# Performance work log

Hardware: AMD Instinct MI355X
Metric: run time of the kernel (lower is better)

The kernel has to match this reference:

```python
import jax, jax.numpy as jnp
import numpy as np


def setup_inputs() -> dict:
    key = jax.random.key(0)
    k1, k2, k3 = jax.random.split(key, 3)
    B, Cin, H, W = 32, 128, 56, 56
    E, Cout = 8, 128
    x = jax.random.normal(k1, (B, Cin, H, W), dtype=jnp.float32)
    conv_w = jax.random.normal(k2, (E, Cout, Cin, 3, 3), dtype=jnp.float32) * 0.05
    gate_w = jax.random.normal(k3, (E, Cin), dtype=jnp.float32) * 0.05
    gate_b = jnp.zeros((E,), dtype=jnp.float32)
    return {"x": x, "conv_w": conv_w, "gate_w": gate_w, "gate_b": gate_b, "top_k": 2}


def reference(x, conv_w, gate_w, gate_b, top_k):
    # x: [B, Cin, H, W]; conv_w: [E, Cout, Cin, 3, 3]
    E, Cout, Cin, kh, kw = conv_w.shape
    B = x.shape[0]
    # Gate: global average pool -> linear logits over experts
    gap = x.mean(axis=(2, 3))                      # [B, Cin]
    logits = gap @ gate_w.T + gate_b               # [B, E]
    vals, idx = jax.lax.top_k(logits, top_k)       # [B, k]
    w = jax.nn.softmax(vals, axis=-1)              # renormalize over selected experts
    weights = jnp.zeros((B, E), dtype=x.dtype).at[jnp.arange(B)[:, None], idx].set(w)
    # All experts via a single conv with stacked output channels (stride=1, pad=1 == SAME)
    y = jax.lax.conv_general_dilated(
        x, conv_w.reshape(E * Cout, Cin, kh, kw),
        window_strides=(1, 1), padding='SAME',
        dimension_numbers=('NCHW', 'OIHW', 'NCHW'))  # [B, E*Cout, H, W]
    y = y.reshape(B, E, Cout, y.shape[2], y.shape[3])
    out = jnp.einsum('be,bechw->bchw', weights, y)  # sparse-weight combine
    return out, weights
```

## Files before the change

### kernel.cpp

```cpp
#include <hip/hip_runtime.h>
#include <hip/hip_bf16.h>

constexpr int Bn   = 32;
constexpr int CIN  = 128;
constexpr int Hh   = 56;
constexpr int Ww   = 56;
constexpr int HW   = Hh * Ww;
constexpr int COUT = 128;
constexpr int En   = 8;

typedef __attribute__((ext_vector_type(8))) short bf16x8;
typedef __attribute__((ext_vector_type(4))) float f32x4;

struct GateInfo { int e0, e1; float w0, w1; };

constexpr size_t ROWB = 58 * 64;
constexpr size_t PGB  = 58 * ROWB;
constexpr int TAPSTR  = COUT * CIN;

constexpr size_t XP_OFF  = 0;
constexpr size_t XP_SZ   = (size_t)Bn * 4 * PGB;
constexpr size_t WW_OFF  = XP_OFF + XP_SZ;
constexpr size_t WW_SZ   = (size_t)Bn * 9 * COUT * CIN * 2;
constexpr size_t HS_OFF  = WW_OFF + WW_SZ;
constexpr size_t HS_SZ   = (size_t)Bn * Hh * CIN * 4;
constexpr size_t GAP_OFF = HS_OFF + HS_SZ;
constexpr size_t GAP_SZ  = (size_t)Bn * CIN * 4;
constexpr size_t GI_OFF  = GAP_OFF + GAP_SZ;

__device__ inline void gload_lds16(const void* g, void* l) {
    __builtin_amdgcn_global_load_lds(
        (const __attribute__((address_space(1))) unsigned int*)g,
        (__attribute__((address_space(3))) unsigned int*)l, 16, 0, 0);
}

__global__ __launch_bounds__(256) void convert_kernel(const float* __restrict__ x,
        char* __restrict__ xpad, float* __restrict__ hsum) {
    __shared__ float lt[CIN * 57];
    int gid = blockIdx.x;
    int b = gid / Hh, h = gid % Hh;
    const float* xp = x + (size_t)b * CIN * HW + h * Ww;
    for (int u = threadIdx.x; u < CIN * Ww; u += 256) {
        int c = u / Ww, w = u % Ww;
        lt[c * 57 + w] = xp[(size_t)c * HW + w];
    }
    __syncthreads();
    char* dst = xpad + (size_t)b * 4 * PGB + (size_t)(h + 1) * ROWB;
    for (int u = threadIdx.x; u < 896; u += 256) {
        int g = u / 224, r = u % 224, w = r >> 2, a = r & 3;
        bf16x8 pk;
        #pragma unroll
        for (int j = 0; j < 8; j++) {
            __hip_bfloat16 t = __float2bfloat16(lt[(g * 32 + a * 8 + j) * 57 + w]);
            pk[j] = *reinterpret_cast<short*>(&t);
        }
        int pq = (a + ((w + 1) >> 1)) & 3;
        *(bf16x8*)(dst + (size_t)g * PGB + (size_t)(w + 1) * 64 + pq * 16) = pk;
    }
    if (threadIdx.x < 32) {
        int t = threadIdx.x, g = t >> 3, side = (t >> 2) & 1, q = t & 3;
        *(int4*)(xpad + (size_t)b * 4 * PGB + (size_t)g * PGB + (size_t)(h + 1) * ROWB
                 + (side ? 57 : 0) * 64 + q * 16) = (int4){0, 0, 0, 0};
    }
    if (h == 0 || h == 55) {
        int row = (h == 0) ? 0 : 57;
        char* base = xpad + (size_t)b * 4 * PGB + (size_t)row * ROWB;
        for (int u = threadIdx.x; u < 928; u += 256) {
            int g = u / 232, r = u % 232;
            *(int4*)(base + (size_t)g * PGB + (size_t)r * 16) = (int4){0, 0, 0, 0};
        }
    }
    if (threadIdx.x < CIN) {
        int c = threadIdx.x;
        float s = 0.f;
        #pragma unroll 8
        for (int w = 0; w < Ww; w++) s += lt[c * 57 + w];
        hsum[((size_t)b * Hh + h) * CIN + c] = s;
    }
}

__global__ __launch_bounds__(128) void gapgate_kernel(const float* __restrict__ hsum,
        const float* __restrict__ gate_w, const float* __restrict__ gate_b,
        float* __restrict__ wout, GateInfo* __restrict__ info) {
    __shared__ float gaps[CIN];
    __shared__ float lg[En];
    __shared__ GateInfo gsh;
    int b = blockIdx.x, tid = threadIdx.x;
    float s = 0.f;
    for (int h = 0; h < Hh; h++) s += hsum[((size_t)b * Hh + h) * CIN + tid];
    gaps[tid] = s * (1.f / (float)HW);
    __syncthreads();
    if (tid < En) {
        float t = gate_b[tid];
        #pragma unroll 8
        for (int c = 0; c < CIN; c++) t += gaps[c] * gate_w[tid * CIN + c];
        lg[tid] = t;
    }
    __syncthreads();
    if (tid == 0) {
        float v[En];
        #pragma unroll
        for (int k = 0; k < En; k++) v[k] = lg[k];
        int i0 = 0; float m0 = v[0];
        #pragma unroll
        for (int k = 1; k < En; k++) if (v[k] > m0) { m0 = v[k]; i0 = k; }
        int i1 = -1; float m1 = -1e30f;
        #pragma unroll
        for (int k = 0; k < En; k++) if (k != i0 && v[k] > m1) { m1 = v[k]; i1 = k; }
        float ex = expf(m1 - m0);
        float den = 1.f + ex;
        GateInfo t; t.e0 = i0; t.e1 = i1; t.w0 = 1.f / den; t.w1 = ex / den;
        gsh = t; info[b] = t;
    }
    __syncthreads();
    if (tid < En) {
        GateInfo t = gsh;
        wout[b * En + tid] = (tid == t.e0) ? t.w0 : (tid == t.e1) ? t.w1 : 0.f;
    }
}

__global__ __launch_bounds__(256) void wcomb_kernel(const float* __restrict__ cw,
        const GateInfo* __restrict__ info, __hip_bfloat16* __restrict__ wws) {
    __shared__ __hip_bfloat16 wl[16 * 1152];
    int b = blockIdx.x >> 3, cg = blockIdx.x & 7;
    GateInfo gi = info[b];
    const float* p0 = cw + (size_t)gi.e0 * COUT * CIN * 9 + (size_t)cg * 16 * 1152;
    const float* p1 = cw + (size_t)gi.e1 * COUT * CIN * 9 + (size_t)cg * 16 * 1152;
    for (int u = threadIdx.x; u < 16 * 1152; u += 256)
        wl[u] = __float2bfloat16(gi.w0 * p0[u] + gi.w1 * p1[u]);
    __syncthreads();
    __hip_bfloat16* wo = wws + (size_t)b * 9 * COUT * CIN + (size_t)cg * 16 * CIN;
    for (int u = threadIdx.x; u < 2304; u += 256) {
        int t = u >> 8, rem = u & 255, co = rem >> 4, a = rem & 15;
        bf16x8 pk;
        #pragma unroll
        for (int j = 0; j < 8; j++)
            pk[j] = *reinterpret_cast<short*>(&wl[co * 1152 + (a * 8 + j) * 9 + t]);
        *(bf16x8*)(wo + (size_t)t * COUT * CIN + co * CIN + a * 8) = pk;
    }
}

__global__ __launch_bounds__(512, 2) void conv_mfma(
        const char* __restrict__ xpad,
        const __hip_bfloat16* __restrict__ wws,
        float* __restrict__ out) {
    __shared__ char xs[2][37120];

    int bid = blockIdx.x;
    int xcd = bid & 7, k = bid >> 3;
    int b   = xcd * 4 + k / 7;
    int rb  = k % 7;
    int row0 = rb * 8;
    int tid = threadIdx.x, wave = tid >> 6, lane = tid & 63;
    int cb = wave >> 2, wq = wave & 3;
    int cout0 = cb * 64;
    int l15 = lane & 15, lk = lane >> 4;

    const char* src = xpad + (size_t)b * 4 * PGB + (size_t)row0 * ROWB;

    int bA[7], bB[7], bC[7];
    #pragma unroll
    for (int i = 0; i < 7; i++) {
        int p = wq * 112 + i * 16 + l15;
        int r = p / 56, m = p % 56;
        int base = r * (int)ROWB + m * 64;
        bA[i] = base + ((lk + (m >> 1)) & 3) * 16;
        bB[i] = base + ((lk + (m >> 1) + 1) & 3) * 16;
        bC[i] = (m & 1) ? bB[i] : bA[i];
    }

    const __hip_bfloat16* ap = wws + (size_t)b * 9 * TAPSTR
                             + (size_t)(cout0 + l15) * CIN + lk * 8;

    f32x4 acc[4][7];
    #pragma unroll
    for (int mt = 0; mt < 4; mt++)
        #pragma unroll
        for (int i = 0; i < 7; i++) acc[mt][i] = (f32x4){0.f, 0.f, 0.f, 0.f};

    bf16x8 areg[3][4];
    #pragma unroll
    for (int mt = 0; mt < 4; mt++)
        areg[0][mt] = *(const bf16x8*)(ap + (size_t)0 * TAPSTR + mt * 16 * CIN);
    #pragma unroll
    for (int mt = 0; mt < 4; mt++)
        areg[1][mt] = *(const bf16x8*)(ap + (size_t)1 * TAPSTR + mt * 16 * CIN);

    #pragma unroll
    for (int kk = 0; kk < 5; kk++) {
        int idx = kk * 512 + tid;
        if (idx < 2320) gload_lds16(src + (size_t)idx * 16, &xs[0][idx * 16]);
    }

    for (int g = 0; g < 4; ++g) {
        __syncthreads();
        if (g < 3) {
            const char* s2 = src + (size_t)(g + 1) * PGB;
            #pragma unroll
            for (int kk = 0; kk < 5; kk++) {
                int idx = kk * 512 + tid;
                if (idx < 2320) gload_lds16(s2 + (size_t)idx * 16, &xs[(g + 1) & 1][idx * 16]);
            }
        }
        const char* xb = xs[g & 1];
        #pragma unroll
        for (int t = 0; t < 9; t++) {
            {
                const int tt = (t < 7) ? t + 2 : t - 7;
                const int gg_add = (t < 7) ? 0 : 1;
                int gg = g + gg_add;
                if (gg < 4) {
                    const __hip_bfloat16* pa = ap + (size_t)tt * TAPSTR + gg * 32;
                    #pragma unroll
                    for (int mt = 0; mt < 4; mt++)
                        areg[(t + 2) % 3][mt] = *(const bf16x8*)(pa + mt * 16 * CIN);
                }
            }
            const int dr = t / 3, dc = t % 3;
            const int imm = dr * (int)ROWB + dc * 64;
            #pragma unroll
            for (int i = 0; i < 7; i++) {
                int boff = (dc == 0) ? bA[i] : (dc == 1) ? bC[i] : bB[i];
                bf16x8 bv = *(const bf16x8*)(xb + boff + imm);
                #pragma unroll
                for (int mt = 0; mt < 4; mt++)
                    acc[mt][i] = __builtin_amdgcn_mfma_f32_16x16x32_bf16(
                        areg[t % 3][mt], bv, acc[mt][i], 0, 0, 0);
            }
        }
    }

    float* outb = out + (size_t)b * COUT * HW + row0 * 56;
    #pragma unroll
    for (int mt = 0; mt < 4; mt++) {
        int cbase = cout0 + mt * 16 + lk * 4;
        #pragma unroll
        for (int i = 0; i < 7; i++) {
            int pp = wq * 112 + i * 16 + l15;
            #pragma unroll
            for (int j = 0; j < 4; j++)
                outb[(size_t)(cbase + j) * HW + pp] = acc[mt][i][j];
        }
    }
}

extern "C" void kernel_launch(void* const* d_in, const int* in_sizes, int n_in,
                              void* d_out, int out_size, void* d_ws, size_t ws_size,
                              hipStream_t stream) {
    const float* x  = (const float*)d_in[0];
    const float* cw = (const float*)d_in[1];
    const float* gw = (const float*)d_in[2];
    const float* gb = (const float*)d_in[3];

    float* out = (float*)d_out;
    char* ws = (char*)d_ws;
    char* xpad           = ws + XP_OFF;
    __hip_bfloat16* wws  = (__hip_bfloat16*)(ws + WW_OFF);
    float* hsum          = (float*)(ws + HS_OFF);
    GateInfo* info       = (GateInfo*)(ws + GI_OFF);
    float* wout = out + (size_t)Bn * COUT * HW;

    convert_kernel<<<Bn * Hh, 256, 0, stream>>>(x, xpad, hsum);
    gapgate_kernel<<<Bn,      128, 0, stream>>>(hsum, gw, gb, wout, info);
    wcomb_kernel  <<<Bn * 8,  256, 0, stream>>>(cw, info, wws);
    conv_mfma     <<<224,     512, 0, stream>>>(xpad, wws, out);
}
```

Before: 168.4 us.

## Stage per-chunk conv weights in LDS instead of per-wave global loads

Weight (A-operand) fragments were loaded directly from global memory by each wave, so the four waves sharing a cout block duplicated those loads. The change has all 512 threads cooperatively load each 32-channel weight chunk into registers, write it to a new 73 KB LDS buffer, and have waves read A fragments from LDS per tap. Global weight traffic per block drops, but LDS use grows from about 74 KB to about 147 KB. That may stop two blocks fitting per CU despite __launch_bounds__(512,2), and it adds nine int4 registers plus an extra barrier per chunk.

```diff
diff --git a/kernel.cpp b/kernel.cpp
--- a/kernel.cpp
+++ b/kernel.cpp
@@ -140,11 +140,13 @@
     }
 }
 
+constexpr int ACH = 9 * COUT * 32 * 2;
 __global__ __launch_bounds__(512, 2) void conv_mfma(
         const char* __restrict__ xpad,
         const __hip_bfloat16* __restrict__ wws,
         float* __restrict__ out) {
     __shared__ char xs[2][37120];
+    __shared__ char als[ACH];
 
     int bid = blockIdx.x;
     int xcd = bid & 7, k = bid >> 3;
@@ -157,6 +159,7 @@
     int l15 = lane & 15, lk = lane >> 4;
 
     const char* src = xpad + (size_t)b * 4 * PGB + (size_t)row0 * ROWB;
+    const __hip_bfloat16* wwb = wws + (size_t)b * 9 * TAPSTR;
 
     int bA[7], bB[7], bC[7];
     #pragma unroll
@@ -169,31 +172,30 @@
         bC[i] = (m & 1) ? bB[i] : bA[i];
     }
 
-    const __hip_bfloat16* ap = wws + (size_t)b * 9 * TAPSTR
-                             + (size_t)(cout0 + l15) * CIN + lk * 8;
-
     f32x4 acc[4][7];
     #pragma unroll
     for (int mt = 0; mt < 4; mt++)
         #pragma unroll
         for (int i = 0; i < 7; i++) acc[mt][i] = (f32x4){0.f, 0.f, 0.f, 0.f};
 
-    bf16x8 areg[3][4];
-    #pragma unroll
-    for (int mt = 0; mt < 4; mt++)
-        areg[0][mt] = *(const bf16x8*)(ap + (size_t)0 * TAPSTR + mt * 16 * CIN);
-    #pragma unroll
-    for (int mt = 0; mt < 4; mt++)
-        areg[1][mt] = *(const bf16x8*)(ap + (size_t)1 * TAPSTR + mt * 16 * CIN);
-
+    int4 areg[9];
+    #pragma unroll
+    for (int kk = 0; kk < 9; kk++) {
+        int n = kk * 512 + tid;
+        int tap = n >> 9, r = n & 511, co = r >> 2, lk8 = (r & 3) * 8;
+        areg[kk] = *(const int4*)(wwb + (size_t)tap * TAPSTR + co * CIN + lk8);
+    }
     #pragma unroll
     for (int kk = 0; kk < 5; kk++) {
         int idx = kk * 512 + tid;
         if (idx < 2320) gload_lds16(src + (size_t)idx * 16, &xs[0][idx * 16]);
     }
+    #pragma unroll
+    for (int kk = 0; kk < 9; kk++)
+        *(int4*)(als + ((size_t)(kk * 512 + tid)) * 16) = areg[kk];
+    __syncthreads();
 
     for (int g = 0; g < 4; ++g) {
-        __syncthreads();
         if (g < 3) {
             const char* s2 = src + (size_t)(g + 1) * PGB;
             #pragma unroll
@@ -201,21 +203,21 @@
                 int idx = kk * 512 + tid;
                 if (idx < 2320) gload_lds16(s2 + (size_t)idx * 16, &xs[(g + 1) & 1][idx * 16]);
             }
+            const int c1 = (g + 1) * 32;
+            #pragma unroll
+            for (int kk = 0; kk < 9; kk++) {
+                int n = kk * 512 + tid;
+                int tap = n >> 9, r = n & 511, co = r >> 2, lk8 = (r & 3) * 8;
+                areg[kk] = *(const int4*)(wwb + (size_t)tap * TAPSTR + co * CIN + c1 + lk8);
+            }
         }
         const char* xb = xs[g & 1];
         #pragma unroll
         for (int t = 0; t < 9; t++) {
-            {
-                const int tt = (t < 7) ? t + 2 : t - 7;
-                const int gg_add = (t < 7) ? 0 : 1;
-                int gg = g + gg_add;
-                if (gg < 4) {
-                    const __hip_bfloat16* pa = ap + (size_t)tt * TAPSTR + gg * 32;
-                    #pragma unroll
-                    for (int mt = 0; mt < 4; mt++)
-                        areg[(t + 2) % 3][mt] = *(const bf16x8*)(pa + mt * 16 * CIN);
-                }
-            }
+            bf16x8 a[4];
+            #pragma unroll
+            for (int mt = 0; mt < 4; mt++)
+                a[mt] = *(const bf16x8*)(als + t * 8192 + (cout0 + mt * 16 + l15) * 64 + lk * 16);
             const int dr = t / 3, dc = t % 3;
             const int imm = dr * (int)ROWB + dc * 64;
             #pragma unroll
@@ -225,9 +227,16 @@
                 #pragma unroll
                 for (int mt = 0; mt < 4; mt++)
                     acc[mt][i] = __builtin_amdgcn_mfma_f32_16x16x32_bf16(
-                        areg[t % 3][mt], bv, acc[mt][i], 0, 0, 0);
+                        a[mt], bv, acc[mt][i], 0, 0, 0);
             }
         }
+        __syncthreads();
+        if (g < 3) {
+            #pragma unroll
+            for (int kk = 0; kk < 9; kk++)
+                *(int4*)(als + ((size_t)(kk * 512 + tid)) * 16) = areg[kk];
+        }
+        __syncthreads();
     }
 
     float* outb = out + (size_t)b * COUT * HW + row0 * 56;
```

New measurement: 168.5 us. No clear change (+0.1%).
